# Kernel optimization log

Measured on AMD Instinct MI355X. Metric: run time of the kernel, lower is better.

## Reference

```python
import jax, jax.numpy as jnp
import numpy as np
import math

C = 256
NUM_GROUPS = 8
EPS = 1e-5


def group_norm(x, scale, bias):
    # x: (B, C, H, W)
    B, Cc, H, W = x.shape
    g = x.reshape(B, NUM_GROUPS, Cc // NUM_GROUPS, H, W)
    mean = g.mean(axis=(2, 3, 4), keepdims=True)
    var = g.var(axis=(2, 3, 4), keepdims=True)
    g = (g - mean) * jax.lax.rsqrt(var + EPS)
    x = g.reshape(B, Cc, H, W)
    return x * scale[None, :, None, None] + bias[None, :, None, None]


def setup_inputs() -> dict:
    key = jax.random.key(0)
    ks = jax.random.split(key, 6)
    B, H, W = 4, 64, 64
    s = 1.0 / math.sqrt(C)
    return {
        "input": jax.random.normal(ks[0], (B, C, H, W), dtype=jnp.float32),
        "gn_scale": jnp.ones((C,), jnp.float32),
        "gn_bias": jnp.zeros((C,), jnp.float32),
        "Wq": jax.random.normal(ks[1], (C, C), jnp.float32) * s,
        "bq": jnp.zeros((C,), jnp.float32),
        "Wk": jax.random.normal(ks[2], (C, C), jnp.float32) * s,
        "bk": jnp.zeros((C,), jnp.float32),
        "Wv": jax.random.normal(ks[3], (C, C), jnp.float32) * s,
        "bv": jnp.zeros((C,), jnp.float32),
        "Wo": jax.random.normal(ks[4], (C, C), jnp.float32) * s,
        "bo": jnp.zeros((C,), jnp.float32),
    }


def reference(input, gn_scale, gn_bias, Wq, bq, Wk, bk, Wv, bv, Wo, bo):
    B, Cc, H, W = input.shape
    N = H * W
    h = group_norm(input, gn_scale, gn_bias)          # (B,C,H,W)
    hf = h.reshape(B, Cc, N)                          # (B,C,N)
    # 1x1 convs are per-pixel linear maps: out[c] = W[c,c'] h[c'] + b[c]
    q = jnp.einsum('oc,bcn->bon', Wq, hf) + bq[None, :, None]
    k = jnp.einsum('oc,bcn->bon', Wk, hf) + bk[None, :, None]
    v = jnp.einsum('oc,bcn->bon', Wv, hf) + bv[None, :, None]
    # attention: scores (B,N,N) = q^T k / sqrt(C)
    attn = jnp.einsum('bcn,bcm->bnm', q, k) / jnp.sqrt(jnp.float32(Cc))
    attn = jax.nn.softmax(attn, axis=-1)
    # output = value @ attention^T -> (B,C,N)
    out = jnp.einsum('bcm,bnm->bcn', v, attn)
    out = out.reshape(B, Cc, H, W)
    out = jnp.einsum('oc,bchw->bohw', Wo, out) + bo[None, :, None, None]
    return input + out
```

## Files before the change

kernel.cpp:

```cpp
#include <hip/hip_runtime.h>
#include <hip/hip_bf16.h>
#include <stdint.h>

#define BATCH 4
#define CH 256
#define NPIX 4096
#define NGROUP 8
#define GCH 32
#define EPSV 1e-5f

typedef __attribute__((ext_vector_type(8))) short bf16x8;
typedef __attribute__((ext_vector_type(4))) float f32x4;
typedef __attribute__((ext_vector_type(16))) float f32x16;

#define MFMA_B16(a, b, c) __builtin_amdgcn_mfma_f32_16x16x32_bf16((a), (b), (c), 0, 0, 0)
#define MFMA32(a, b, c)   __builtin_amdgcn_mfma_f32_32x32x16_bf16((a), (b), (c), 0, 0, 0)

#define GLOAD16(gsrc, ldst)                                                        \
  __builtin_amdgcn_global_load_lds(                                               \
      (const __attribute__((address_space(1))) uint32_t*)(gsrc),                  \
      (__attribute__((address_space(3))) uint32_t*)(ldst), 16, 0, 0)

__device__ __forceinline__ unsigned short f2bf(float f) {
  union { float f; uint32_t u; } v; v.f = f;
  return (unsigned short)((v.u + 0x7FFFu + ((v.u >> 16) & 1u)) >> 16);
}
__device__ __forceinline__ float bf2f(unsigned short h) {
  union { uint32_t u; float f; } v; v.u = ((uint32_t)h) << 16;
  return v.f;
}

#define QSCALE 0.09016813306f

__global__ __launch_bounds__(256) void wconv(
    const float* __restrict__ Wq, const float* __restrict__ Wk,
    const float* __restrict__ Wv, const float* __restrict__ Wo,
    const float* __restrict__ bq,
    unsigned short* __restrict__ Wq_b, unsigned short* __restrict__ Wk_b,
    unsigned short* __restrict__ Wv_b, unsigned short* __restrict__ Wo_b,
    float* __restrict__ bq_s) {
  int i = blockIdx.x * 256 + threadIdx.x;
  Wq_b[i] = f2bf(Wq[i] * QSCALE);
  Wk_b[i] = f2bf(Wk[i]);
  Wv_b[i] = f2bf(Wv[i]);
  Wo_b[i] = f2bf(Wo[i]);
  if (i < CH) bq_s[i] = bq[i] * QSCALE;
}

__global__ __launch_bounds__(256) void gn_stats(const float* __restrict__ x,
                                                float* __restrict__ part) {
  int bc = blockIdx.x;
  const float* row = x + (size_t)bc * NPIX;
  int t = threadIdx.x;
  float s = 0.f, ss = 0.f;
  #pragma unroll
  for (int i = 0; i < 4; ++i) {
    f32x4 v = *(const f32x4*)(row + (i * 256 + t) * 4);
    s += v[0] + v[1] + v[2] + v[3];
    ss += v[0]*v[0] + v[1]*v[1] + v[2]*v[2] + v[3]*v[3];
  }
  #pragma unroll
  for (int m = 1; m < 64; m <<= 1) { s += __shfl_xor(s, m); ss += __shfl_xor(ss, m); }
  __shared__ float ls[8];
  if ((t & 63) == 0) { ls[(t >> 6) * 2] = s; ls[(t >> 6) * 2 + 1] = ss; }
  __syncthreads();
  if (t == 0) {
    part[bc * 2]     = ls[0] + ls[2] + ls[4] + ls[6];
    part[bc * 2 + 1] = ls[1] + ls[3] + ls[5] + ls[7];
  }
}

__global__ __launch_bounds__(256) void gn_apply(
    const float* __restrict__ x, const float* __restrict__ part,
    const float* __restrict__ gamma, const float* __restrict__ beta,
    unsigned short* __restrict__ h_t) {
  int chunk = blockIdx.x, g = blockIdx.y, b = blockIdx.z;
  int t = threadIdx.x;
  __shared__ float s_mean, s_rstd;
  __shared__ unsigned short tile[GCH][72];
  if (t == 0) {
    float S = 0.f, SS = 0.f;
    const float* p = part + (size_t)(b * CH + g * GCH) * 2;
    for (int j = 0; j < GCH; ++j) { S += p[2 * j]; SS += p[2 * j + 1]; }
    float inv = 1.0f / (float)(GCH * NPIX);
    float mean = S * inv;
    float var = SS * inv - mean * mean;
    s_mean = mean;
    s_rstd = rsqrtf(var + EPSV);
  }
  __syncthreads();
  float mean = s_mean, rstd = s_rstd;
  int n0 = chunk * 64;
  int p = t & 63;
  int csub = t >> 6;
  #pragma unroll
  for (int cl = 0; cl < GCH; cl += 4) {
    int c = cl + csub;
    float val = x[(size_t)(b * CH + g * GCH + c) * NPIX + n0 + p];
    float gm = gamma[g * GCH + c], bt = beta[g * GCH + c];
    tile[c][p] = f2bf((val - mean) * rstd * gm + bt);
  }
  __syncthreads();
  int pix = t >> 2, cc = (t & 3) * 8;
  bf16x8 vv;
  #pragma unroll
  for (int j = 0; j < 8; ++j) vv[j] = (short)tile[cc + j][pix];
  *(bf16x8*)(h_t + (size_t)(b * NPIX + n0 + pix) * CH + g * GCH + cc) = vv;
}

template <int BIAS_COL, int RESID, int OUT_BF16>
__global__ __launch_bounds__(256, 2) void gemm_bt_k(
    const unsigned short* __restrict__ A, const unsigned short* __restrict__ Bt,
    void* __restrict__ Cout, const float* __restrict__ bias,
    const float* __restrict__ resid, int M, int N,
    long aStride, long btStride, long cStride) {
  __shared__ __align__(16) unsigned short a_lds[128 * 64];
  __shared__ __align__(16) unsigned short b_lds[128 * 64];

  const int bz = blockIdx.z;
  const char* Ac = (const char*)(A + (size_t)bz * aStride);
  const char* Bc = (const char*)(Bt + (size_t)bz * btStride);
  const int m0 = blockIdx.x * 128;
  const int n0 = blockIdx.y * 128;
  const int t = threadIdx.x;
  const int w = t >> 6, l = t & 63, lr = l & 15, lk = l >> 4;
  const int wr = (w >> 1) * 64, wc = (w & 1) * 64;

  f32x4 acc[4][4];
  #pragma unroll
  for (int i = 0; i < 4; ++i)
    #pragma unroll
    for (int j = 0; j < 4; ++j) acc[i][j] = f32x4{0.f, 0.f, 0.f, 0.f};

  char* alc = (char*)a_lds;
  char* blc = (char*)b_lds;

  for (int kt = 0; kt < 4; ++kt) {
    __syncthreads();
    #pragma unroll
    for (int i = 0; i < 4; ++i) {
      int base = i * 4096 + w * 1024;
      int lin = base + l * 16;
      int sw = lin ^ (((lin >> 7) & 7) << 4);
      int row = lin >> 7;
      int inr = sw & 127;
      GLOAD16(Ac + (size_t)(m0 + row) * 512 + kt * 128 + inr, alc + base);
      GLOAD16(Bc + (size_t)(n0 + row) * 512 + kt * 128 + inr, blc + base);
    }
    __syncthreads();
    #pragma unroll
    for (int ks = 0; ks < 2; ++ks) {
      bf16x8 af[4], bf[4];
      #pragma unroll
      for (int f = 0; f < 4; ++f) {
        int ra = wr + f * 16 + lr;
        int la = ra * 128 + ks * 64 + lk * 16;
        af[f] = *(const bf16x8*)(alc + (la ^ ((ra & 7) << 4)));
        int rb = wc + f * 16 + lr;
        int lb = rb * 128 + ks * 64 + lk * 16;
        bf[f] = *(const bf16x8*)(blc + (lb ^ ((rb & 7) << 4)));
      }
      #pragma unroll
      for (int mf = 0; mf < 4; ++mf)
        #pragma unroll
        for (int nf = 0; nf < 4; ++nf)
          acc[mf][nf] = MFMA_B16(af[mf], bf[nf], acc[mf][nf]);
    }
  }

  #pragma unroll
  for (int mf = 0; mf < 4; ++mf) {
    #pragma unroll
    for (int nf = 0; nf < 4; ++nf) {
      int col = n0 + wc + nf * 16 + lr;
      #pragma unroll
      for (int r = 0; r < 4; ++r) {
        int row = m0 + wr + mf * 16 + lk * 4 + r;
        float val = acc[mf][nf][r];
        val += BIAS_COL ? bias[col] : bias[row];
        size_t idx = (size_t)bz * (size_t)cStride + (size_t)row * N + col;
        if (RESID) val += resid[idx];
        if (OUT_BF16) ((unsigned short*)Cout)[idx] = f2bf(val);
        else          ((float*)Cout)[idx] = val;
      }
    }
  }
}

#define KSPLIT 4
#define KRANGE (NPIX / KSPLIT)
#define KBLK 32
#define NT (KRANGE / KBLK)

__global__ __launch_bounds__(256, 2) void flash_kernel(
    const unsigned short* __restrict__ q_t, const unsigned short* __restrict__ k_t,
    const unsigned short* __restrict__ v,
    unsigned short* __restrict__ p0, unsigned short* __restrict__ p1,
    unsigned short* __restrict__ p2, unsigned short* __restrict__ p3,
    float* __restrict__ ml) {
  __shared__ __align__(16) unsigned short k_lds[2][KBLK * CH];
  __shared__ __align__(16) unsigned short v_lds[2][CH * KBLK];

  const int F = blockIdx.x;
  const int bid = (F >> 3) + ((F & 7) << 6);
  const int qx = bid & 31, b = (bid >> 5) & 3, ksp = bid >> 7;
  const int q0 = qx * 128;
  const int t = threadIdx.x;
  const int w = t >> 6, l = t & 63;
  const int l31 = l & 31, hi = l >> 5;

  bf16x8 qf[16];
  {
    const char* qp = (const char*)(q_t + (size_t)(b * NPIX + q0 + w * 32 + l31) * CH);
    #pragma unroll
    for (int ds = 0; ds < 16; ++ds)
      qf[ds] = *(const bf16x8*)(qp + ds * 32 + hi * 16);
  }

  f32x16 oacc[8];
  #pragma unroll
  for (int cf = 0; cf < 8; ++cf)
    #pragma unroll
    for (int r = 0; r < 16; ++r) oacc[cf][r] = 0.f;
  float m_run = -3e38f, l_run = 0.f;

  const char* kg = (const char*)(k_t + ((size_t)b * NPIX + ksp * KRANGE) * CH);
  const char* vg = (const char*)(v + (size_t)b * CH * NPIX + ksp * KRANGE);

  #define STAGE(buf, tt)                                                           \
    {                                                                              \
      _Pragma("unroll")                                                            \
      for (int i_ = 0; i_ < 4; ++i_) {                                             \
        int d = i_ * 4096 + w * 1024 + l * 16;                                     \
        int r_ = d >> 9, c_ = ((d >> 4) & 31) ^ r_;                                \
        GLOAD16(kg + (size_t)((tt) * KBLK + r_) * 512 + (c_ << 4),                 \
                (char*)k_lds[buf] + d);                                            \
      }                                                                            \
      _Pragma("unroll")                                                            \
      for (int i_ = 0; i_ < 4; ++i_) {                                             \
        int d = i_ * 4096 + w * 1024 + l * 16;                                     \
        int r_ = d >> 9, c5 = ((d >> 4) & 31) ^ r_;                                \
        GLOAD16(vg + (size_t)((c5 >> 2) * 32 + r_) * (NPIX * 2) +                  \
                    (size_t)(tt) * (KBLK * 2) + ((c5 & 3) << 4),                   \
                (char*)v_lds[buf] + d);                                            \
      }                                                                            \
    }

  STAGE(0, 0);
  STAGE(1, 1);
  asm volatile("s_waitcnt vmcnt(8)" ::: "memory");
  __builtin_amdgcn_s_barrier();

  int cur = 0;
  for (int it = 0; it < NT; ++it) {
    const char* klc = (const char*)k_lds[cur];
    const char* vlc = (const char*)v_lds[cur];

    f32x16 s0, s1;
    #pragma unroll
    for (int r = 0; r < 16; ++r) { s0[r] = 0.f; s1[r] = 0.f; }
    __builtin_amdgcn_s_setprio(1);
    #pragma unroll
    for (int ds = 0; ds < 16; ++ds) {
      bf16x8 kf = *(const bf16x8*)(klc + l31 * 512 + ((((ds << 1) + hi) ^ l31) << 4));
      if (ds & 1) s1 = MFMA32(kf, qf[ds], s1);
      else        s0 = MFMA32(kf, qf[ds], s0);
    }
    __builtin_amdgcn_s_setprio(0);
    #pragma unroll
    for (int r = 0; r < 16; ++r) s0[r] += s1[r];

    float t8[8];
    #pragma unroll
    for (int r = 0; r < 8; ++r) t8[r] = fmaxf(s0[r], s0[r + 8]);
    float ta = fmaxf(fmaxf(t8[0], t8[4]), fmaxf(t8[1], t8[5]));
    float tb = fmaxf(fmaxf(t8[2], t8[6]), fmaxf(t8[3], t8[7]));
    float tm = fmaxf(ta, tb);
    tm = fmaxf(tm, __shfl_xor(tm, 32));

    if (!__all(tm <= m_run + 6.f)) {
      float mn = fmaxf(m_run, tm);
      float al = exp2f(m_run - mn);
      m_run = mn;
      l_run *= al;
      #pragma unroll
      for (int r = 0; r < 16; ++r) {
        float alr = __shfl(al, (r & 3) + 8 * (r >> 2) + 4 * hi);
        #pragma unroll
        for (int cf = 0; cf < 8; ++cf) oacc[cf][r] *= alr;
      }
    }

    float ps = 0.f;
    uint32_t pk[8];
    #pragma unroll
    for (int m = 0; m < 8; ++m) {
      float pa = exp2f(s0[2 * m] - m_run);
      float pb = exp2f(s0[2 * m + 1] - m_run);
      ps += pa + pb;
      union { __hip_bfloat162 h2; uint32_t u; } cv;
      cv.h2 = __float22bfloat162_rn(make_float2(pa, pb));
      pk[m] = cv.u;
    }
    ps += __shfl_xor(ps, 32);
    l_run += ps;

    __builtin_amdgcn_s_setprio(1);
    #pragma unroll
    for (int s = 0; s < 2; ++s) {
      uint32_t own0 = hi ? pk[4 * s + 2] : pk[4 * s + 0];
      uint32_t own1 = hi ? pk[4 * s + 3] : pk[4 * s + 1];
      uint32_t snd0 = hi ? pk[4 * s + 0] : pk[4 * s + 2];
      uint32_t snd1 = hi ? pk[4 * s + 1] : pk[4 * s + 3];
      uint32_t rcv0 = (uint32_t)__shfl_xor((int)snd0, 32);
      uint32_t rcv1 = (uint32_t)__shfl_xor((int)snd1, 32);
      union { uint32_t u[4]; bf16x8 v8; } apu;
      apu.u[0] = hi ? rcv0 : own0;
      apu.u[1] = hi ? rcv1 : own1;
      apu.u[2] = hi ? own0 : rcv0;
      apu.u[3] = hi ? own1 : rcv1;
      bf16x8 ap = apu.v8;
      #pragma unroll
      for (int cf = 0; cf < 8; ++cf) {
        bf16x8 bv = *(const bf16x8*)(
            vlc + l31 * 512 + ((((cf << 2) + (s << 1) + hi) ^ l31) << 4));
        oacc[cf] = MFMA32(ap, bv, oacc[cf]);
      }
    }
    __builtin_amdgcn_s_setprio(0);

    asm volatile("" ::: "memory");
    __builtin_amdgcn_s_barrier();
    if (it + 2 < NT) STAGE(cur, it + 2);
    asm volatile("s_waitcnt vmcnt(8)" ::: "memory");
    __builtin_amdgcn_s_barrier();
    cur ^= 1;
  }

  {
    unsigned short* opart = (ksp == 0) ? p0 : (ksp == 1) ? p1 : (ksp == 2) ? p2 : p3;
    unsigned short* op = opart + (size_t)(b * NPIX + q0 + w * 32) * CH;
    #pragma unroll
    for (int cf = 0; cf < 8; ++cf)
      #pragma unroll
      for (int r = 0; r < 16; ++r)
        op[(size_t)((r & 3) + 8 * (r >> 2) + 4 * hi) * CH + cf * 32 + l31] =
            f2bf(oacc[cf][r]);
    if (l < 32) {
      float* mlrow = ml + ((size_t)ksp * (BATCH * NPIX) +
                           b * NPIX + q0 + w * 32 + l) * 2;
      mlrow[0] = m_run;
      mlrow[1] = l_run;
    }
  }
}

__global__ __launch_bounds__(256) void flash_merge(
    const unsigned short* __restrict__ p0, unsigned short* __restrict__ p1io,
    const unsigned short* __restrict__ p2, const unsigned short* __restrict__ p3,
    const float* __restrict__ ml) {
  const int R = BATCH * NPIX;
  int t = threadIdx.x;
  int gr = blockIdx.x * 16 + (t >> 4);
  int colg = (t & 15) * 16;
  float m0 = ml[(size_t)gr * 2],           l0 = ml[(size_t)gr * 2 + 1];
  float m1 = ml[((size_t)R + gr) * 2],     l1 = ml[((size_t)R + gr) * 2 + 1];
  float m2 = ml[((size_t)2 * R + gr) * 2], l2 = ml[((size_t)2 * R + gr) * 2 + 1];
  float m3 = ml[((size_t)3 * R + gr) * 2], l3 = ml[((size_t)3 * R + gr) * 2 + 1];
  float m = fmaxf(fmaxf(m0, m1), fmaxf(m2, m3));
  float e0 = exp2f(m0 - m), e1 = exp2f(m1 - m);
  float e2 = exp2f(m2 - m), e3 = exp2f(m3 - m);
  float inv = 1.0f / (e0 * l0 + e1 * l1 + e2 * l2 + e3 * l3);
  const bf16x8* a0 = (const bf16x8*)(p0 + (size_t)gr * CH + colg);
  bf16x8*       a1 = (bf16x8*)(p1io + (size_t)gr * CH + colg);
  const bf16x8* a2 = (const bf16x8*)(p2 + (size_t)gr * CH + colg);
  const bf16x8* a3 = (const bf16x8*)(p3 + (size_t)gr * CH + colg);
  #pragma unroll
  for (int h = 0; h < 2; ++h) {
    bf16x8 v0 = a0[h], v1 = a1[h], v2 = a2[h], v3 = a3[h], o;
    #pragma unroll
    for (int j = 0; j < 8; ++j)
      o[j] = (short)f2bf((e0 * bf2f((unsigned short)v0[j]) +
                          e1 * bf2f((unsigned short)v1[j]) +
                          e2 * bf2f((unsigned short)v2[j]) +
                          e3 * bf2f((unsigned short)v3[j])) * inv);
    a1[h] = o;
  }
}

extern "C" void kernel_launch(void* const* d_in, const int* in_sizes, int n_in,
                              void* d_out, int out_size, void* d_ws, size_t ws_size,
                              hipStream_t stream) {
  const float* x   = (const float*)d_in[0];
  const float* gsc = (const float*)d_in[1];
  const float* gbi = (const float*)d_in[2];
  const float* Wq  = (const float*)d_in[3];
  const float* bq  = (const float*)d_in[4];
  const float* Wk  = (const float*)d_in[5];
  const float* bk  = (const float*)d_in[6];
  const float* Wv  = (const float*)d_in[7];
  const float* bv  = (const float*)d_in[8];
  const float* Wo  = (const float*)d_in[9];
  const float* bo  = (const float*)d_in[10];

  char* ws = (char*)d_ws;
  unsigned short* Wq_b = (unsigned short*)(ws);
  unsigned short* Wk_b = (unsigned short*)(ws + 131072);
  unsigned short* Wv_b = (unsigned short*)(ws + 262144);
  unsigned short* Wo_b = (unsigned short*)(ws + 393216);
  float* bq_s          = (float*)(ws + 524288);
  float* part          = (float*)(ws + 525312);
  char* big            = ws + 533504;
  unsigned short* h_t  = (unsigned short*)(big);
  unsigned short* q_t  = (unsigned short*)(big + 1 * 8388608ull);
  unsigned short* k_t  = (unsigned short*)(big + 2 * 8388608ull);
  unsigned short* v_   = (unsigned short*)(big + 3 * 8388608ull);
  unsigned short* o_t  = (unsigned short*)(big + 4 * 8388608ull);
  float* ml            = (float*)(big + 5 * 8388608ull);
  if (ws_size < 533504 + 5ull * 8388608ull + 524288ull) return;

  unsigned short* dout_u = (unsigned short*)d_out;
  unsigned short* op2 = dout_u;
  unsigned short* op3 = dout_u + 4194304;

  wconv<<<256, 256, 0, stream>>>(Wq, Wk, Wv, Wo, bq, Wq_b, Wk_b, Wv_b, Wo_b, bq_s);
  gn_stats<<<BATCH * CH, 256, 0, stream>>>(x, part);
  gn_apply<<<dim3(64, NGROUP, BATCH), 256, 0, stream>>>(x, part, gsc, gbi, h_t);

  gemm_bt_k<1, 0, 1><<<dim3(128, 2, 1), 256, 0, stream>>>(
      h_t, Wq_b, q_t, bq_s, nullptr, 16384, 256, 0, 0, 0);
  gemm_bt_k<1, 0, 1><<<dim3(128, 2, 1), 256, 0, stream>>>(
      h_t, Wk_b, k_t, bk, nullptr, 16384, 256, 0, 0, 0);
  gemm_bt_k<0, 0, 1><<<dim3(2, 32, BATCH), 256, 0, stream>>>(
      Wv_b, h_t, v_, bv, nullptr, 256, 4096, 0, 1048576, 1048576);

  flash_kernel<<<dim3(32 * BATCH * KSPLIT, 1, 1), 256, 0, stream>>>(
      q_t, k_t, v_, h_t, o_t, op2, op3, ml);
  flash_merge<<<(BATCH * NPIX) / 16, 256, 0, stream>>>(h_t, o_t, op2, op3, ml);

  gemm_bt_k<0, 1, 0><<<dim3(2, 32, BATCH), 256, 0, stream>>>(
      Wo_b, o_t, (float*)d_out, bo, x, 256, 4096, 0, 1048576, 1048576);
}
```

Measured before the change: 170.7 us.

## Software-pipeline flash attention: overlap previous tile's PV MFMAs with current QK

Restructures the attention inner loop so that the P·V matmul for tile u-1 is issued together with the Q·K matmul for tile u. K is staged two tiles ahead and V one tile behind, with separate staging macros and waitcnt depths adjusted at the tail. The goal is to hide the softmax/exp latency behind MFMA work. It also precomputes global/LDS load offsets, uses a single score accumulator and tree reductions for the max and sum. This keeps the packed P registers live across iterations, which raises register pressure.

```diff
diff --git a/kernel.cpp b/kernel.cpp
--- a/kernel.cpp
+++ b/kernel.cpp
@@ -223,95 +223,42 @@
     #pragma unroll
     for (int r = 0; r < 16; ++r) oacc[cf][r] = 0.f;
   float m_run = -3e38f, l_run = 0.f;
+  uint32_t pkc[8];
+  #pragma unroll
+  for (int m = 0; m < 8; ++m) pkc[m] = 0;
 
   const char* kg = (const char*)(k_t + ((size_t)b * NPIX + ksp * KRANGE) * CH);
   const char* vg = (const char*)(v + (size_t)b * CH * NPIX + ksp * KRANGE);
 
-  #define STAGE(buf, tt)                                                           \
-    {                                                                              \
-      _Pragma("unroll")                                                            \
-      for (int i_ = 0; i_ < 4; ++i_) {                                             \
-        int d = i_ * 4096 + w * 1024 + l * 16;                                     \
-        int r_ = d >> 9, c_ = ((d >> 4) & 31) ^ r_;                                \
-        GLOAD16(kg + (size_t)((tt) * KBLK + r_) * 512 + (c_ << 4),                 \
-                (char*)k_lds[buf] + d);                                            \
-      }                                                                            \
-      _Pragma("unroll")                                                            \
-      for (int i_ = 0; i_ < 4; ++i_) {                                             \
-        int d = i_ * 4096 + w * 1024 + l * 16;                                     \
-        int r_ = d >> 9, c5 = ((d >> 4) & 31) ^ r_;                                \
-        GLOAD16(vg + (size_t)((c5 >> 2) * 32 + r_) * (NPIX * 2) +                  \
-                    (size_t)(tt) * (KBLK * 2) + ((c5 & 3) << 4),                   \
-                (char*)v_lds[buf] + d);                                            \
-      }                                                                            \
-    }
-
-  STAGE(0, 0);
-  STAGE(1, 1);
-  asm volatile("s_waitcnt vmcnt(8)" ::: "memory");
-  __builtin_amdgcn_s_barrier();
-
-  int cur = 0;
-  for (int it = 0; it < NT; ++it) {
-    const char* klc = (const char*)k_lds[cur];
-    const char* vlc = (const char*)v_lds[cur];
-
-    f32x16 s0, s1;
-    #pragma unroll
-    for (int r = 0; r < 16; ++r) { s0[r] = 0.f; s1[r] = 0.f; }
-    __builtin_amdgcn_s_setprio(1);
-    #pragma unroll
-    for (int ds = 0; ds < 16; ++ds) {
-      bf16x8 kf = *(const bf16x8*)(klc + l31 * 512 + ((((ds << 1) + hi) ^ l31) << 4));
-      if (ds & 1) s1 = MFMA32(kf, qf[ds], s1);
-      else        s0 = MFMA32(kf, qf[ds], s0);
-    }
-    __builtin_amdgcn_s_setprio(0);
-    #pragma unroll
-    for (int r = 0; r < 16; ++r) s0[r] += s1[r];
-
-    float t8[8];
-    #pragma unroll
-    for (int r = 0; r < 8; ++r) t8[r] = fmaxf(s0[r], s0[r + 8]);
-    float ta = fmaxf(fmaxf(t8[0], t8[4]), fmaxf(t8[1], t8[5]));
-    float tb = fmaxf(fmaxf(t8[2], t8[6]), fmaxf(t8[3], t8[7]));
-    float tm = fmaxf(ta, tb);
-    tm = fmaxf(tm, __shfl_xor(tm, 32));
-
-    if (!__all(tm <= m_run + 6.f)) {
-      float mn = fmaxf(m_run, tm);
-      float al = exp2f(m_run - mn);
-      m_run = mn;
-      l_run *= al;
-      #pragma unroll
-      for (int r = 0; r < 16; ++r) {
-        float alr = __shfl(al, (r & 3) + 8 * (r >> 2) + 4 * hi);
-        #pragma unroll
-        for (int cf = 0; cf < 8; ++cf) oacc[cf][r] *= alr;
-      }
-    }
-
-    float ps = 0.f;
-    uint32_t pk[8];
-    #pragma unroll
-    for (int m = 0; m < 8; ++m) {
-      float pa = exp2f(s0[2 * m] - m_run);
-      float pb = exp2f(s0[2 * m + 1] - m_run);
-      ps += pa + pb;
-      union { __hip_bfloat162 h2; uint32_t u; } cv;
-      cv.h2 = __float22bfloat162_rn(make_float2(pa, pb));
-      pk[m] = cv.u;
-    }
-    ps += __shfl_xor(ps, 32);
-    l_run += ps;
-
-    __builtin_amdgcn_s_setprio(1);
+  int koffb[4], voffb[4], ldsd[4];
+  #pragma unroll
+  for (int i_ = 0; i_ < 4; ++i_) {
+    int d = i_ * 4096 + w * 1024 + l * 16;
+    ldsd[i_] = d;
+    int r_ = d >> 9;
+    int c_ = ((d >> 4) & 31) ^ r_;
+    koffb[i_] = r_ * 512 + (c_ << 4);
+    voffb[i_] = ((c_ >> 2) * 32 + r_) * (NPIX * 2) + ((c_ & 3) << 4);
+  }
+
+  #define STAGE_K(buf, tt)                                                         \
+    { _Pragma("unroll")                                                            \
+      for (int i_ = 0; i_ < 4; ++i_)                                               \
+        GLOAD16(kg + (size_t)koffb[i_] + (size_t)(tt) * (KBLK * 512),              \
+                (char*)k_lds[buf] + ldsd[i_]); }
+  #define STAGE_V(buf, tt)                                                         \
+    { _Pragma("unroll")                                                            \
+      for (int i_ = 0; i_ < 4; ++i_)                                               \
+        GLOAD16(vg + (size_t)voffb[i_] + (size_t)(tt) * (KBLK * 2),                \
+                (char*)v_lds[buf] + ldsd[i_]); }
+
+  auto do_pv = [&](const char* vlcx) {
     #pragma unroll
     for (int s = 0; s < 2; ++s) {
-      uint32_t own0 = hi ? pk[4 * s + 2] : pk[4 * s + 0];
-      uint32_t own1 = hi ? pk[4 * s + 3] : pk[4 * s + 1];
-      uint32_t snd0 = hi ? pk[4 * s + 0] : pk[4 * s + 2];
-      uint32_t snd1 = hi ? pk[4 * s + 1] : pk[4 * s + 3];
+      uint32_t own0 = hi ? pkc[4 * s + 2] : pkc[4 * s + 0];
+      uint32_t own1 = hi ? pkc[4 * s + 3] : pkc[4 * s + 1];
+      uint32_t snd0 = hi ? pkc[4 * s + 0] : pkc[4 * s + 2];
+      uint32_t snd1 = hi ? pkc[4 * s + 1] : pkc[4 * s + 3];
       uint32_t rcv0 = (uint32_t)__shfl_xor((int)snd0, 32);
       uint32_t rcv1 = (uint32_t)__shfl_xor((int)snd1, 32);
       union { uint32_t u[4]; bf16x8 v8; } apu;
@@ -323,19 +270,84 @@
       #pragma unroll
       for (int cf = 0; cf < 8; ++cf) {
         bf16x8 bv = *(const bf16x8*)(
-            vlc + l31 * 512 + ((((cf << 2) + (s << 1) + hi) ^ l31) << 4));
+            vlcx + l31 * 512 + ((((cf << 2) + (s << 1) + hi) ^ l31) << 4));
         oacc[cf] = MFMA32(ap, bv, oacc[cf]);
       }
     }
+  };
+
+  STAGE_K(0, 0);
+  STAGE_K(1, 1);
+  STAGE_V(0, 0);
+  asm volatile("s_waitcnt vmcnt(8)" ::: "memory");
+  __builtin_amdgcn_s_barrier();
+
+  for (int u = 0; u < NT; ++u) {
+    const char* klc = (const char*)k_lds[u & 1];
+    const char* vlc = (const char*)v_lds[(u ^ 1) & 1];
+
+    __builtin_amdgcn_s_setprio(1);
+    if (u > 0) do_pv(vlc);
+    f32x16 sacc;
+    #pragma unroll
+    for (int r = 0; r < 16; ++r) sacc[r] = 0.f;
+    #pragma unroll
+    for (int ds = 0; ds < 16; ++ds) {
+      bf16x8 kf = *(const bf16x8*)(klc + l31 * 512 + ((((ds << 1) + hi) ^ l31) << 4));
+      sacc = MFMA32(kf, qf[ds], sacc);
+    }
     __builtin_amdgcn_s_setprio(0);
+
+    float mx[8];
+    #pragma unroll
+    for (int r = 0; r < 8; ++r) mx[r] = fmaxf(sacc[r], sacc[r + 8]);
+    #pragma unroll
+    for (int st = 4; st >= 1; st >>= 1)
+      #pragma unroll
+      for (int r = 0; r < 4; ++r)
+        if (r < st) mx[r] = fmaxf(mx[r], mx[r + st]);
+    float tm = fmaxf(mx[0], __shfl_xor(mx[0], 32));
+
+    if (!__all(tm <= m_run + 6.f)) {
+      float mn = fmaxf(m_run, tm);
+      float al = exp2f(m_run - mn);
+      m_run = mn;
+      l_run *= al;
+      #pragma unroll
+      for (int r = 0; r < 16; ++r) {
+        float alr = __shfl(al, (r & 3) + 8 * (r >> 2) + 4 * hi);
+        #pragma unroll
+        for (int cf = 0; cf < 8; ++cf) oacc[cf][r] *= alr;
+      }
+    }
+
+    float psp[4] = {0.f, 0.f, 0.f, 0.f};
+    #pragma unroll
+    for (int m = 0; m < 8; ++m) {
+      float pa = exp2f(sacc[2 * m] - m_run);
+      float pb = exp2f(sacc[2 * m + 1] - m_run);
+      psp[m & 3] += pa + pb;
+      union { __hip_bfloat162 h2; uint32_t u; } cv;
+      cv.h2 = __float22bfloat162_rn(make_float2(pa, pb));
+      pkc[m] = cv.u;
+    }
+    float ps = (psp[0] + psp[1]) + (psp[2] + psp[3]);
+    ps += __shfl_xor(ps, 32);
+    l_run += ps;
 
     asm volatile("" ::: "memory");
     __builtin_amdgcn_s_barrier();
-    if (it + 2 < NT) STAGE(cur, it + 2);
-    asm volatile("s_waitcnt vmcnt(8)" ::: "memory");
+    if (u + 2 < NT) STAGE_K((u & 1), u + 2);
+    if (u + 1 < NT) STAGE_V(((u + 1) & 1), u + 1);
+    if (u + 2 < NT)      { asm volatile("s_waitcnt vmcnt(8)" ::: "memory"); }
+    else if (u + 1 < NT) { asm volatile("s_waitcnt vmcnt(4)" ::: "memory"); }
+    else                 { asm volatile("s_waitcnt vmcnt(0)" ::: "memory"); }
     __builtin_amdgcn_s_barrier();
-    cur ^= 1;
-  }
+  }
+
+  __builtin_amdgcn_s_setprio(1);
+  do_pv((const char*)v_lds[(NT - 1) & 1]);
+  __builtin_amdgcn_s_setprio(0);
 
   {
     unsigned short* opart = (ksp == 0) ? p0 : (ksp == 1) ? p1 : (ksp == 2) ? p2 : p3;
@@ -353,6 +365,8 @@
       mlrow[1] = l_run;
     }
   }
+  #undef STAGE_K
+  #undef STAGE_V
 }
 
 __global__ __launch_bounds__(256) void flash_merge(
```

Result: faster. 146.7 us (-14.1%).
